# Kernel tuning notes

Measured on AMD Instinct MI355X. Metric: run time of the kernel, lower is better.

## Reference

```python
import jax, jax.numpy as jnp
import numpy as np

B, S, D_IN, D_OUT, BLK = 2, 2048, 4096, 16384, 32
NBLK = D_IN // BLK  # 128


def setup_inputs() -> dict:
    key = jax.random.key(0)
    k_x, k_q, k_s, k_b = jax.random.split(key, 4)
    x = jax.random.normal(k_x, (B, S, D_IN), dtype=jnp.float32)
    # GGML Q8_0: signed 8-bit quants per block of 32
    qs = jax.random.randint(k_q, (D_OUT, NBLK, BLK), -128, 128, dtype=jnp.int32)
    # per-block scales (stand-in for the fp16 'd' field); small magnitude
    scales = jax.random.uniform(k_s, (D_OUT, NBLK), dtype=jnp.float32) * 0.02
    bias = jax.random.normal(k_b, (D_OUT,), dtype=jnp.float32)
    return {"x": x, "qs": qs, "scales": scales, "bias": bias}


def reference(x, qs, scales, bias):
    # _materialize_weight: block dequantize (d * q per block) then cast to input dtype
    # qs: [O, NBLK, BLK], scales: [O, NBLK] -> W: [O, D_IN]
    W = (scales[:, :, None] * qs.astype(x.dtype)).reshape(D_OUT, D_IN)
    # host Linear: y = x @ W^T + b
    y = jnp.einsum('bsd,od->bso', x, W) + bias
    return y
```

## Files before the change

### kernel.cpp

```cpp
#include <hip/hip_runtime.h>
#include <cstdint>
#include <cstddef>

#define M_DIM 4096
#define N_DIM 16384
#define K_DIM 4096
#define NBLK_Q 128

#define BM 256
#define BN 256
#define BK 32
#define KSTEPS (K_DIM / BK)
#define BUFB 16384
#define NBUF 4

typedef int i32x4 __attribute__((ext_vector_type(4)));
typedef int i32x16 __attribute__((ext_vector_type(16)));

#define SFENCE() __builtin_amdgcn_sched_barrier(0)
#define BAR() __builtin_amdgcn_s_barrier()
#define WAITVM(n) asm volatile("s_waitcnt vmcnt(" #n ")")
#define WAITLG0() asm volatile("s_waitcnt lgkmcnt(0)")

__global__ __launch_bounds__(256) void prep(
    const float* __restrict__ x, const int* __restrict__ qs,
    const float* __restrict__ scales, char* __restrict__ A8S,
    char* __restrict__ B8S, float* __restrict__ sxr, float* __restrict__ swc) {
  if (blockIdx.x < M_DIM) {
    const int m = blockIdx.x;
    const int t = threadIdx.x;
    const float* xr = x + (size_t)m * K_DIM + t * 16;
    float4 v[4];
#pragma unroll
    for (int i = 0; i < 4; ++i) v[i] = ((const float4*)xr)[i];
    float amax = 0.f;
#pragma unroll
    for (int i = 0; i < 4; ++i)
      amax = fmaxf(amax, fmaxf(fmaxf(fabsf(v[i].x), fabsf(v[i].y)),
                               fmaxf(fabsf(v[i].z), fabsf(v[i].w))));
#pragma unroll
    for (int off = 32; off; off >>= 1) amax = fmaxf(amax, __shfl_xor(amax, off, 64));
    __shared__ float wmax[4];
    if ((t & 63) == 0) wmax[t >> 6] = amax;
    __syncthreads();
    amax = fmaxf(fmaxf(wmax[0], wmax[1]), fmaxf(wmax[2], wmax[3]));
    const float inv = 127.0f / amax;
    if (t == 0) sxr[m] = amax / 127.0f;
    unsigned d[4];
#pragma unroll
    for (int i = 0; i < 4; ++i) {
      int q0 = (int)rintf(v[i].x * inv), q1 = (int)rintf(v[i].y * inv);
      int q2 = (int)rintf(v[i].z * inv), q3 = (int)rintf(v[i].w * inv);
      d[i] = (q0 & 0xff) | ((q1 & 0xff) << 8) | ((q2 & 0xff) << 16) | ((q3 & 0xff) << 24);
    }
    const int k32 = t >> 1, kg = t & 1;
    const int mtile = m >> 8, mm = m & 255, m32 = mm >> 5, r = mm & 31;
    int4* dst = (int4*)(A8S + ((size_t)(mtile * 128 + k32)) * 8192 + m32 * 1024 + kg * 512 + r * 16);
    *dst = make_int4(d[0], d[1], d[2], d[3]);
  } else {
    const int o = (blockIdx.x - M_DIM) * 4 + (threadIdx.x >> 6);
    const int l = threadIdx.x & 63;
    const float s0 = scales[(size_t)o * NBLK_Q + l];
    const float s1 = scales[(size_t)o * NBLK_Q + 64 + l];
    float S = fmaxf(s0, s1);
#pragma unroll
    for (int off = 32; off; off >>= 1) S = fmaxf(S, __shfl_xor(S, off, 64));
    if (l == 0) swc[o] = S;
    const float rS = 1.0f / S;
    const int nt = o >> 8, col = o & 255, n32 = col >> 5, c = col & 31;
#pragma unroll
    for (int h = 0; h < 2; ++h) {
      const int nb = l + 64 * h;
      const float ratio = ((h == 0) ? s0 : s1) * rS;
      const int4* q = (const int4*)(qs + ((size_t)o * NBLK_Q + nb) * 32);
      unsigned d[8];
#pragma unroll
      for (int g = 0; g < 8; ++g) {
        int4 v = q[g];
        int a0 = (int)rintf((float)v.x * ratio);
        int a1 = (int)rintf((float)v.y * ratio);
        int a2 = (int)rintf((float)v.z * ratio);
        int a3 = (int)rintf((float)v.w * ratio);
        d[g] = (a0 & 0xff) | ((a1 & 0xff) << 8) | ((a2 & 0xff) << 16) | ((a3 & 0xff) << 24);
      }
      char* dst = B8S + ((size_t)(nt * 128 + nb)) * 8192 + n32 * 1024 + c * 16;
      ((int4*)dst)[0] = make_int4(d[0], d[1], d[2], d[3]);
      ((int4*)(dst + 512))[0] = make_int4(d[4], d[5], d[6], d[7]);
    }
  }
}

__global__ __launch_bounds__(512, 2) void gemm_i8(
    const char* __restrict__ A8S, const char* __restrict__ B8S,
    const float* __restrict__ sxr, const float* __restrict__ swc,
    const float* __restrict__ bias, float* __restrict__ C) {
  __shared__ __align__(16) char lds[NBUF * BUFB];

  const int tid = threadIdx.x;
  const int w = tid >> 6;
  const int l = tid & 63;
  const int wm = w >> 2;
  const int wn = w & 3;

  const int bid = blockIdx.x;
  const int xcd = bid & 7;
  const int k = bid >> 3;
  const int mtile = xcd * 2 + (k & 1);
  const int ntile = k >> 1;
  const int brow = mtile * BM;
  const int bcol = ntile * BN;

  const char* srcA = A8S + (size_t)mtile * 128 * 8192 + w * 1024 + l * 16;
  const char* srcB = B8S + (size_t)ntile * 128 * 8192 + w * 1024 + l * 16;
  const int doffA = w * 1024 + l * 16;
  const int doffB = 8192 + w * 1024 + l * 16;
  const int roffA = wm * 4096 + l * 16;
  const int roffB = 8192 + wn * 2048 + l * 16;

  i32x16 acc[4][2] = {};
  i32x4 a0[4], b0[2], a1[4], b1[2];
  int4 gA0, gB0, gA1, gB1;

  {
    int4 ta0 = *(const int4*)(srcA);
    int4 tb0 = *(const int4*)(srcB);
    int4 ta1 = *(const int4*)(srcA + 8192);
    int4 tb1 = *(const int4*)(srcB + 8192);
    *(int4*)(lds + doffA) = ta0;
    *(int4*)(lds + doffB) = tb0;
    *(int4*)(lds + BUFB + doffA) = ta1;
    *(int4*)(lds + BUFB + doffB) = tb1;
    gA0 = *(const int4*)(srcA + 2 * 8192);
    gB0 = *(const int4*)(srcB + 2 * 8192);
    WAITLG0();
    SFENCE(); BAR(); SFENCE();
#pragma unroll
    for (int i = 0; i < 4; ++i)
      a0[i] = *(const i32x4*)(lds + roffA + i * 1024);
#pragma unroll
    for (int j = 0; j < 2; ++j)
      b0[j] = *(const i32x4*)(lds + roffB + j * 1024);
  }

#define STEP(KT, CA, CB, NA, NB, WA, WB, LA, LB)                               \
  do {                                                                         \
    const char* rb = lds + (((KT) + 1) & 3) * BUFB;                            \
    NA[0] = *(const i32x4*)(rb + roffA);                                       \
    NA[1] = *(const i32x4*)(rb + roffA + 1024);                                \
    NA[2] = *(const i32x4*)(rb + roffA + 2048);                                \
    NA[3] = *(const i32x4*)(rb + roffA + 3072);                                \
    NB[0] = *(const i32x4*)(rb + roffB);                                       \
    NB[1] = *(const i32x4*)(rb + roffB + 1024);                                \
    {                                                                          \
      const int ql = ((KT) + 3 > KSTEPS - 1) ? (KSTEPS - 1) : ((KT) + 3);      \
      LA = *(const int4*)(srcA + (size_t)ql * 8192);                           \
      LB = *(const int4*)(srcB + (size_t)ql * 8192);                           \
    }                                                                          \
    SFENCE();                                                                  \
    __builtin_amdgcn_s_setprio(1);                                             \
    acc[0][0] = __builtin_amdgcn_mfma_i32_32x32x32_i8(CA[0], CB[0], acc[0][0], 0, 0, 0); \
    acc[0][1] = __builtin_amdgcn_mfma_i32_32x32x32_i8(CA[0], CB[1], acc[0][1], 0, 0, 0); \
    acc[1][0] = __builtin_amdgcn_mfma_i32_32x32x32_i8(CA[1], CB[0], acc[1][0], 0, 0, 0); \
    acc[1][1] = __builtin_amdgcn_mfma_i32_32x32x32_i8(CA[1], CB[1], acc[1][1], 0, 0, 0); \
    acc[2][0] = __builtin_amdgcn_mfma_i32_32x32x32_i8(CA[2], CB[0], acc[2][0], 0, 0, 0); \
    acc[2][1] = __builtin_amdgcn_mfma_i32_32x32x32_i8(CA[2], CB[1], acc[2][1], 0, 0, 0); \
    acc[3][0] = __builtin_amdgcn_mfma_i32_32x32x32_i8(CA[3], CB[0], acc[3][0], 0, 0, 0); \
    acc[3][1] = __builtin_amdgcn_mfma_i32_32x32x32_i8(CA[3], CB[1], acc[3][1], 0, 0, 0); \
    __builtin_amdgcn_s_setprio(0);                                             \
    SFENCE();                                                                  \
    WAITVM(2);                                                                 \
    {                                                                          \
      char* wb = lds + (((KT) + 2) & 3) * BUFB;                                \
      *(int4*)(wb + doffA) = WA;                                               \
      *(int4*)(wb + doffB) = WB;                                               \
    }                                                                          \
    SFENCE();                                                                  \
    WAITLG0();                                                                 \
    SFENCE(); BAR(); SFENCE();                                                 \
  } while (0)

  for (int kt = 0; kt < KSTEPS; kt += 2) {
    STEP(kt, a0, b0, a1, b1, gA0, gB0, gA1, gB1);
    STEP(kt + 1, a1, b1, a0, b0, gA1, gB1, gA0, gB0);
  }
#undef STEP

#pragma unroll
  for (int i = 0; i < 4; ++i) {
    const int rb = brow + wm * 128 + i * 32 + 4 * (l >> 5);
#pragma unroll
    for (int j = 0; j < 2; ++j) {
      const int col = bcol + wn * 64 + j * 32 + (l & 31);
      const float Sw = swc[col];
      const float bv = bias[col];
#pragma unroll
      for (int r = 0; r < 16; ++r) {
        const int row = rb + (r & 3) + 8 * (r >> 2);
        C[(size_t)row * N_DIM + col] = (float)acc[i][j][r] * (sxr[row] * Sw) + bv;
      }
    }
  }
}

__global__ void naive_gemm(const float* __restrict__ x, const int* __restrict__ qs,
                           const float* __restrict__ scales, const float* __restrict__ bias,
                           float* __restrict__ y) {
  size_t idx = (size_t)blockIdx.x * 256 + threadIdx.x;
  if (idx >= (size_t)M_DIM * N_DIM) return;
  int o = (int)(idx % N_DIM);
  size_t m = idx / N_DIM;
  const float* xr = x + m * K_DIM;
  const int* q = qs + (size_t)o * K_DIM;
  const float* sc = scales + (size_t)o * NBLK_Q;
  float sum = 0.f;
  for (int nb = 0; nb < NBLK_Q; ++nb) {
    float s = sc[nb];
    float bs = 0.f;
#pragma unroll 8
    for (int b = 0; b < 32; ++b) bs += xr[nb * 32 + b] * (float)q[nb * 32 + b];
    sum += s * bs;
  }
  y[idx] = sum + bias[o];
}

extern "C" void kernel_launch(void* const* d_in, const int* in_sizes, int n_in,
                              void* d_out, int out_size, void* d_ws, size_t ws_size,
                              hipStream_t stream) {
  const float* x = (const float*)d_in[0];
  const int* qs = (const int*)d_in[1];
  const float* scales = (const float*)d_in[2];
  const float* bias = (const float*)d_in[3];
  float* y = (float*)d_out;

  const size_t A8_bytes = (size_t)M_DIM * K_DIM;
  const size_t B8_bytes = (size_t)N_DIM * K_DIM;
  const size_t SX_bytes = (size_t)M_DIM * 4;
  const size_t SW_bytes = (size_t)N_DIM * 4;

  if (ws_size < A8_bytes + B8_bytes + SX_bytes + SW_bytes) {
    size_t total = (size_t)M_DIM * N_DIM;
    naive_gemm<<<(unsigned)((total + 255) / 256), 256, 0, stream>>>(x, qs, scales, bias, y);
    return;
  }

  char* A8S = (char*)d_ws;
  char* B8S = A8S + A8_bytes;
  float* sxr = (float*)(B8S + B8_bytes);
  float* swc = (float*)((char*)sxr + SX_bytes);

  prep<<<M_DIM + N_DIM / 4, 256, 0, stream>>>(x, qs, scales, A8S, B8S, sxr, swc);
  gemm_i8<<<(M_DIM / BM) * (N_DIM / BN), 512, 0, stream>>>(A8S, B8S, sxr, swc, bias, y);
}
```

Baseline: 424.0 us.

## Split weight requantization into scale pass and LDS-staged coalesced packing kernel

Weight prep now happens in two steps. First, per-row scale ratios are computed once and written transposed into a workspace buffer. Then a new kernel assigns each block one (n-tile, k-block) pair, requantizes 256 rows' 32 quants into LDS and writes the 8 KB packed tile contiguously, so the B8S stores are coalesced. It adds one extra kernel launch, an 8 MB ratio buffer round trip, and strided global reads of qs (each thread reads 128 contiguous bytes from a different row).

```diff
diff --git a/kernel.cpp b/kernel.cpp
--- a/kernel.cpp
+++ b/kernel.cpp
@@ -22,10 +22,10 @@
 #define WAITVM(n) asm volatile("s_waitcnt vmcnt(" #n ")")
 #define WAITLG0() asm volatile("s_waitcnt lgkmcnt(0)")
 
-__global__ __launch_bounds__(256) void prep(
-    const float* __restrict__ x, const int* __restrict__ qs,
-    const float* __restrict__ scales, char* __restrict__ A8S,
-    char* __restrict__ B8S, float* __restrict__ sxr, float* __restrict__ swc) {
+__global__ __launch_bounds__(256) void prep_a(
+    const float* __restrict__ x, const float* __restrict__ scales,
+    char* __restrict__ A8S, float* __restrict__ sxr,
+    float* __restrict__ swc, float* __restrict__ ratioT) {
   if (blockIdx.x < M_DIM) {
     const int m = blockIdx.x;
     const int t = threadIdx.x;
@@ -58,36 +58,56 @@
     int4* dst = (int4*)(A8S + ((size_t)(mtile * 128 + k32)) * 8192 + m32 * 1024 + kg * 512 + r * 16);
     *dst = make_int4(d[0], d[1], d[2], d[3]);
   } else {
-    const int o = (blockIdx.x - M_DIM) * 4 + (threadIdx.x >> 6);
-    const int l = threadIdx.x & 63;
-    const float s0 = scales[(size_t)o * NBLK_Q + l];
-    const float s1 = scales[(size_t)o * NBLK_Q + 64 + l];
-    float S = fmaxf(s0, s1);
-#pragma unroll
-    for (int off = 32; off; off >>= 1) S = fmaxf(S, __shfl_xor(S, off, 64));
-    if (l == 0) swc[o] = S;
+    const int o = (blockIdx.x - M_DIM) * 256 + threadIdx.x;
+    const float4* sp = (const float4*)(scales + (size_t)o * NBLK_Q);
+    float4 sc[32];
+#pragma unroll
+    for (int i = 0; i < 32; ++i) sc[i] = sp[i];
+    float S = 0.f;
+#pragma unroll
+    for (int i = 0; i < 32; ++i)
+      S = fmaxf(S, fmaxf(fmaxf(sc[i].x, sc[i].y), fmaxf(sc[i].z, sc[i].w)));
+    swc[o] = S;
     const float rS = 1.0f / S;
-    const int nt = o >> 8, col = o & 255, n32 = col >> 5, c = col & 31;
-#pragma unroll
-    for (int h = 0; h < 2; ++h) {
-      const int nb = l + 64 * h;
-      const float ratio = ((h == 0) ? s0 : s1) * rS;
-      const int4* q = (const int4*)(qs + ((size_t)o * NBLK_Q + nb) * 32);
-      unsigned d[8];
-#pragma unroll
-      for (int g = 0; g < 8; ++g) {
-        int4 v = q[g];
-        int a0 = (int)rintf((float)v.x * ratio);
-        int a1 = (int)rintf((float)v.y * ratio);
-        int a2 = (int)rintf((float)v.z * ratio);
-        int a3 = (int)rintf((float)v.w * ratio);
-        d[g] = (a0 & 0xff) | ((a1 & 0xff) << 8) | ((a2 & 0xff) << 16) | ((a3 & 0xff) << 24);
-      }
-      char* dst = B8S + ((size_t)(nt * 128 + nb)) * 8192 + n32 * 1024 + c * 16;
-      ((int4*)dst)[0] = make_int4(d[0], d[1], d[2], d[3]);
-      ((int4*)(dst + 512))[0] = make_int4(d[4], d[5], d[6], d[7]);
+#pragma unroll
+    for (int i = 0; i < 32; ++i) {
+      ratioT[(size_t)(4 * i + 0) * N_DIM + o] = sc[i].x * rS;
+      ratioT[(size_t)(4 * i + 1) * N_DIM + o] = sc[i].y * rS;
+      ratioT[(size_t)(4 * i + 2) * N_DIM + o] = sc[i].z * rS;
+      ratioT[(size_t)(4 * i + 3) * N_DIM + o] = sc[i].w * rS;
     }
   }
+}
+
+__global__ __launch_bounds__(256) void pack_w8t(
+    const int* __restrict__ qs, const float* __restrict__ ratioT,
+    char* __restrict__ B8S) {
+  __shared__ __align__(16) char tile[8192];
+  const int bid = blockIdx.x;
+  const int nt = bid >> 7;
+  const int k32 = bid & 127;
+  const int t = threadIdx.x;
+  const int o = nt * 256 + t;
+
+  const float ratio = ratioT[(size_t)k32 * N_DIM + o];
+  const int4* q = (const int4*)(qs + ((size_t)o * NBLK_Q + k32) * 32);
+  unsigned d[8];
+#pragma unroll
+  for (int g = 0; g < 8; ++g) {
+    int4 v = q[g];
+    int a0 = (int)rintf((float)v.x * ratio);
+    int a1 = (int)rintf((float)v.y * ratio);
+    int a2 = (int)rintf((float)v.z * ratio);
+    int a3 = (int)rintf((float)v.w * ratio);
+    d[g] = (a0 & 0xff) | ((a1 & 0xff) << 8) | ((a2 & 0xff) << 16) | ((a3 & 0xff) << 24);
+  }
+  const int n32 = t >> 5, c = t & 31;
+  *(int4*)(tile + n32 * 1024 + c * 16) = make_int4(d[0], d[1], d[2], d[3]);
+  *(int4*)(tile + n32 * 1024 + 512 + c * 16) = make_int4(d[4], d[5], d[6], d[7]);
+  __syncthreads();
+  char* dst = B8S + (size_t)(nt * 128 + k32) * 8192;
+  *(int4*)(dst + t * 16) = *(const int4*)(tile + t * 16);
+  *(int4*)(dst + 4096 + t * 16) = *(const int4*)(tile + 4096 + t * 16);
 }
 
 __global__ __launch_bounds__(512, 2) void gemm_i8(
@@ -236,8 +256,9 @@
   const size_t B8_bytes = (size_t)N_DIM * K_DIM;
   const size_t SX_bytes = (size_t)M_DIM * 4;
   const size_t SW_bytes = (size_t)N_DIM * 4;
-
-  if (ws_size < A8_bytes + B8_bytes + SX_bytes + SW_bytes) {
+  const size_t RT_bytes = (size_t)NBLK_Q * N_DIM * 4;
+
+  if (ws_size < A8_bytes + B8_bytes + SX_bytes + SW_bytes + RT_bytes) {
     size_t total = (size_t)M_DIM * N_DIM;
     naive_gemm<<<(unsigned)((total + 255) / 256), 256, 0, stream>>>(x, qs, scales, bias, y);
     return;
@@ -247,7 +268,9 @@
   char* B8S = A8S + A8_bytes;
   float* sxr = (float*)(B8S + B8_bytes);
   float* swc = (float*)((char*)sxr + SX_bytes);
-
-  prep<<<M_DIM + N_DIM / 4, 256, 0, stream>>>(x, qs, scales, A8S, B8S, sxr, swc);
+  float* ratioT = (float*)((char*)swc + SW_bytes);
+
+  prep_a<<<M_DIM + N_DIM / 256, 256, 0, stream>>>(x, scales, A8S, sxr, swc, ratioT);
+  pack_w8t<<<(N_DIM / 256) * NBLK_Q, 256, 0, stream>>>(qs, ratioT, B8S);
   gemm_i8<<<(M_DIM / BM) * (N_DIM / BN), 512, 0, stream>>>(A8S, B8S, sxr, swc, bias, y);
 }
```

New measurement: 428.2 us. No clear change (+1.0%).
